# Kernel tuning notes

Measured on AMD Instinct MI355X. Metric: run time of the kernel, lower is better.

## Reference

```python
import jax, jax.numpy as jnp
import numpy as np

D_MODEL = 1024
NHEAD = 16
HEAD_DIM = D_MODEL // NHEAD


def setup_inputs() -> dict:
    key = jax.random.key(0)
    ks = jax.random.split(key, 7)
    N, S, E = 2, 2048, D_MODEL
    query = jax.random.normal(ks[0], (N, S, E), dtype=jnp.float32)
    key_t = jax.random.normal(ks[1], (N, S, E), dtype=jnp.float32)
    value = jax.random.normal(ks[2], (N, S, E), dtype=jnp.float32)
    # nn.Linear default init scale ~ 1/sqrt(fan_in)
    s = 1.0 / np.sqrt(E)
    w_in = jax.random.uniform(ks[3], (3 * E, E), jnp.float32, -s, s)
    b_in = jax.random.uniform(ks[4], (3 * E,), jnp.float32, -s, s)
    w_o = jax.random.uniform(ks[5], (E, E), jnp.float32, -s, s)
    b_o = jax.random.uniform(ks[6], (E,), jnp.float32, -s, s)
    return {"query": query, "key": key_t, "value": value,
            "w_in": w_in, "b_in": b_in, "w_o": w_o, "b_o": b_o}


def reference(query, key, value, w_in, b_in, w_o, b_o):
    # NOTE: the torch module computes q,k,v all from `query` (self-attention);
    # the `key`/`value` args are ignored by its forward math.
    N, S, E = query.shape
    H, Dh = NHEAD, HEAD_DIM
    qkv = query @ w_in.T + b_in                      # (N, S, 3E)
    q, k, v = jnp.split(qkv, 3, axis=-1)
    def heads(x):
        return x.reshape(N, S, H, Dh).transpose(0, 2, 1, 3)  # (N, H, S, Dh)
    q, k, v = heads(q), heads(k), heads(v)
    scale = 1.0 / jnp.sqrt(jnp.asarray(Dh, query.dtype))
    scores = jnp.einsum('bhqd,bhkd->bhqk', q, k) * scale     # (N, H, S, S)
    attn = jax.nn.softmax(scores, axis=-1)
    out = jnp.einsum('bhqk,bhkd->bhqd', attn, v)             # (N, H, S, Dh)
    out = out.transpose(0, 2, 1, 3).reshape(N, S, E)
    return out @ w_o.T + b_o
```

## Files before the change

### kernel.cpp

```cpp
#include <hip/hip_runtime.h>
#include <hip/hip_bf16.h>
#include <stdint.h>

#define NB   2
#define SEQ  2048
#define EMB  1024
#define NH   16
#define DH   64
#define MR   (NB*SEQ)
#define E3   (3*EMB)
#define CSC  (0.125f * 1.44269504f)

typedef __attribute__((ext_vector_type(8))) short bf16x8;
typedef __attribute__((ext_vector_type(4))) float f32x4;
typedef __attribute__((ext_vector_type(16))) float f32x16;

__device__ __forceinline__ unsigned short f2bf(float f) {
  unsigned u = __float_as_uint(f);
  unsigned r = (u + 0x7FFF + ((u >> 16) & 1)) >> 16;
  return (unsigned short)r;
}
__device__ __forceinline__ unsigned pack2(float lo, float hi) {
  return (unsigned)f2bf(lo) | ((unsigned)f2bf(hi) << 16);
}
__device__ __forceinline__ float bf2f(unsigned short s) {
  return __uint_as_float(((unsigned)s) << 16);
}
__device__ __forceinline__ unsigned cvtpk(float lo, float hi) {
  unsigned r;
  asm("v_cvt_pk_bf16_f32 %0, %1, %2" : "=v"(r) : "v"(lo), "v"(hi));
  return r;
}

__device__ __forceinline__ void gld16(const unsigned short* g, unsigned short* l) {
  __builtin_amdgcn_global_load_lds(
      (const __attribute__((address_space(1))) unsigned int*)g,
      (__attribute__((address_space(3))) unsigned int*)l,
      16, 0, 0);
}

__global__ void cvt_all(const float* __restrict__ q,
                        const float* __restrict__ w_in,
                        const float* __restrict__ w_o,
                        unsigned short* __restrict__ Xbf,
                        unsigned short* __restrict__ Winbf,
                        unsigned short* __restrict__ Wobf) {
  int b = blockIdx.x;
  const float* src; unsigned short* dst; int off;
  if (b < 2048)      { src = q;    dst = Xbf;   off = b; }
  else if (b < 3584) { src = w_in; dst = Winbf; off = b - 2048; }
  else               { src = w_o;  dst = Wobf;  off = b - 3584; }
  int i = (off * 256 + threadIdx.x) * 8;
  float4 a = *(const float4*)(src + i);
  float4 c = *(const float4*)(src + i + 4);
  uint4 o;
  o.x = pack2(a.x, a.y);
  o.y = pack2(a.z, a.w);
  o.z = pack2(c.x, c.y);
  o.w = pack2(c.z, c.w);
  *(uint4*)(dst + i) = o;
}

template<int BN, bool OUT_F32>
__global__ __launch_bounds__(256) void gemm_bt(
    const unsigned short* __restrict__ A,
    const unsigned short* __restrict__ Bt,
    const float* __restrict__ bias,
    void* __restrict__ Cout,
    int K, int ldc, int scale_cols) {
  constexpr int NR = BN / 32;
  constexpr int WNT = BN / 2;
  __shared__ unsigned short As[4096];
  __shared__ unsigned short Bs[BN * 32];
  const int tid  = threadIdx.x;
  const int lane = tid & 63;
  const int w    = tid >> 6;
  const int wm = w >> 1, wn = w & 1;
  const int g = lane >> 4, li = lane & 15;
  const int rowBase = blockIdx.x * 128;
  const int colBase = blockIdx.y * BN;

  f32x4 acc[4][NR];
#pragma unroll
  for (int m = 0; m < 4; ++m)
#pragma unroll
    for (int nn = 0; nn < NR; ++nn) { acc[m][nn][0]=0.f; acc[m][nn][1]=0.f; acc[m][nn][2]=0.f; acc[m][nn][3]=0.f; }

  const unsigned short* Ag = A  + (size_t)(rowBase + (tid >> 2)) * K + (tid & 3) * 8;
  const unsigned short* Bg = Bt + (size_t)(colBase + (tid >> 2)) * K + (tid & 3) * 8;

  for (int k0 = 0; k0 < K; k0 += 32) {
    __syncthreads();
    gld16(Ag + k0,                As + tid * 8);
    gld16(Ag + (size_t)64*K + k0, As + 2048 + tid * 8);
    gld16(Bg + k0,                Bs + tid * 8);
    if (BN == 128)
      gld16(Bg + (size_t)64*K + k0, Bs + 2048 + tid * 8);
    __syncthreads();

    bf16x8 af[4], bfv[NR];
#pragma unroll
    for (int m = 0; m < 4; ++m)
      af[m] = *(const bf16x8*)&As[(wm*64 + m*16 + li) * 32 + g * 8];
#pragma unroll
    for (int nn = 0; nn < NR; ++nn)
      bfv[nn] = *(const bf16x8*)&Bs[(wn*WNT + nn*16 + li) * 32 + g * 8];
#pragma unroll
    for (int m = 0; m < 4; ++m)
#pragma unroll
      for (int nn = 0; nn < NR; ++nn)
        acc[m][nn] = __builtin_amdgcn_mfma_f32_16x16x32_bf16(af[m], bfv[nn], acc[m][nn], 0, 0, 0);
  }

#pragma unroll
  for (int nn = 0; nn < NR; ++nn) {
    const int col = colBase + wn*WNT + nn*16 + li;
    const float bv = bias[col];
    const float sc = (col < scale_cols) ? CSC : 1.0f;
#pragma unroll
    for (int m = 0; m < 4; ++m) {
      const int r0 = rowBase + wm*64 + m*16 + g*4;
#pragma unroll
      for (int r = 0; r < 4; ++r) {
        float v = (acc[m][nn][r] + bv) * sc;
        if (OUT_F32) ((float*)Cout)[(size_t)(r0 + r) * ldc + col] = v;
        else ((unsigned short*)Cout)[(size_t)(r0 + r) * ldc + col] = f2bf(v);
      }
    }
  }
}

__global__ __launch_bounds__(256, 3) void attn32(
    const unsigned short* __restrict__ qkv,
    unsigned short* __restrict__ O0,
    unsigned short* __restrict__ O1,
    float* __restrict__ ML) {
  __shared__ unsigned short smem[16384];
  char* LB = (char*)smem;

  const int tid  = threadIdx.x;
  const int lane = tid & 63;
  const int w    = tid >> 6;
  const int hi   = lane >> 5;
  const int l31  = lane & 31;
  const int slot = blockIdx.x;
  const int bid  = (slot & 7) * 128 + (slot >> 3);
  const int qb = bid & 15, h = (bid >> 4) & 15, n = (bid >> 8) & 1, z = bid >> 9;
  const size_t rowN = (size_t)n * SEQ;
  const int kt0 = z * 1024;
  const int vp_ = tid & 31, dblk = tid >> 5;
  const int vps = (vp_ & ~6) | ((vp_ & 2) << 1) | ((vp_ & 4) >> 1);
  unsigned short* Oz = z ? O1 : O0;

  bf16x8 qf[4];
  {
    const size_t qr = rowN + qb*128 + w*32 + l31;
#pragma unroll
    for (int kc = 0; kc < 4; ++kc)
      qf[kc] = *(const bf16x8*)&qkv[qr * E3 + h*64 + kc*16 + hi*8];
  }

  f32x16 ZEROV;
#pragma unroll
  for (int i = 0; i < 16; ++i) ZEROV[i] = 0.f;
  f32x16 acc0 = ZEROV, acc1 = ZEROV;
  float ssum[8];
#pragma unroll
  for (int i = 0; i < 8; ++i) ssum[i] = 0.f;

  uint4 pv0, pv1;
  auto stageK = [&](int kt, int buf) {
#pragma unroll
    for (int p = 0; p < 2; ++p) {
      int r = p*32 + (tid >> 3);
      int ch = (tid & 7) ^ (r & 7);
      gld16(&qkv[(rowN + kt + r) * E3 + EMB + h*64 + ch*8],
            &smem[buf*4096 + p*2048 + tid*8]);
    }
  };
  auto loadV = [&](int kt) {
    const unsigned short* vp = &qkv[(rowN + kt + 2*vp_) * E3 + 2*EMB + h*64 + dblk*8];
    pv0 = *(const uint4*)vp;
    pv1 = *(const uint4*)(vp + E3);
  };
  auto writeV = [&](int buf) {
    const unsigned short* s0 = (const unsigned short*)&pv0;
    const unsigned short* s1 = (const unsigned short*)&pv1;
#pragma unroll
    for (int j = 0; j < 8; ++j) {
      int d = dblk*8 + j;
      unsigned val = (unsigned)s0[j] | ((unsigned)s1[j] << 16);
      *(unsigned*)(LB + 16384 + buf*8192 + d*128 + (((vps>>2) ^ (d&7)) << 4) + (vps&3)*4) = val;
    }
  };

  loadV(kt0);
  stageK(kt0, 0);
  writeV(0);
  __syncthreads();

  for (int t = 0; t < 16; ++t) {
    const int cur = t & 1;
    const bool pre = (t + 1 < 16);
    const int ktn = kt0 + (t + 1) * 64;
    if (pre) { loadV(ktn); stageK(ktn, cur^1); }

    const char* Kb = LB + cur*8192;
    bf16x8 ka[4], kb[4];
#pragma unroll
    for (int kc = 0; kc < 4; ++kc) {
      const int sw = ((kc*2 + hi) ^ (l31 & 7)) << 4;
      ka[kc] = *(const bf16x8*)(Kb + l31*128 + sw);
      kb[kc] = *(const bf16x8*)(Kb + 4096 + l31*128 + sw);
    }
    __builtin_amdgcn_s_setprio(1);
    f32x16 z0 = __builtin_amdgcn_mfma_f32_32x32x16_bf16(ka[0], qf[0], ZEROV, 0, 0, 0);
    f32x16 z1 = __builtin_amdgcn_mfma_f32_32x32x16_bf16(kb[0], qf[0], ZEROV, 0, 0, 0);
#pragma unroll
    for (int kc = 1; kc < 4; ++kc) {
      z0 = __builtin_amdgcn_mfma_f32_32x32x16_bf16(ka[kc], qf[kc], z0, 0, 0, 0);
      z1 = __builtin_amdgcn_mfma_f32_32x32x16_bf16(kb[kc], qf[kc], z1, 0, 0, 0);
    }
    __builtin_amdgcn_s_setprio(0);

#pragma unroll
    for (int i = 0; i < 16; ++i) {
      z0[i] = __builtin_amdgcn_exp2f(z0[i]);
      z1[i] = __builtin_amdgcn_exp2f(z1[i]);
    }
#pragma unroll
    for (int i = 0; i < 8; ++i)
      ssum[i] += (z0[2*i] + z0[2*i+1]) + (z1[2*i] + z1[2*i+1]);

    bf16x8 pf[4];
    {
      union { bf16x8 v; unsigned u[4]; } r0_, r1_, r2_, r3_;
#pragma unroll
      for (int j = 0; j < 4; ++j) {
        r0_.u[j] = cvtpk(z0[2*j],     z0[2*j + 1]);
        r1_.u[j] = cvtpk(z0[8 + 2*j], z0[9 + 2*j]);
        r2_.u[j] = cvtpk(z1[2*j],     z1[2*j + 1]);
        r3_.u[j] = cvtpk(z1[8 + 2*j], z1[9 + 2*j]);
      }
      pf[0] = r0_.v; pf[1] = r1_.v; pf[2] = r2_.v; pf[3] = r3_.v;
    }

    if (pre) writeV(cur ^ 1);

    const char* Vb = LB + 16384 + cur*8192;
    __builtin_amdgcn_s_setprio(1);
#pragma unroll
    for (int c = 0; c < 4; ++c) {
      const int sw = ((c*2 + hi) ^ (l31 & 7)) << 4;
      bf16x8 va = *(const bf16x8*)(Vb + l31*128 + sw);
      bf16x8 vb = *(const bf16x8*)(Vb + 4096 + l31*128 + sw);
      acc0 = __builtin_amdgcn_mfma_f32_32x32x16_bf16(va, pf[c], acc0, 0, 0, 0);
      acc1 = __builtin_amdgcn_mfma_f32_32x32x16_bf16(vb, pf[c], acc1, 0, 0, 0);
    }
    __builtin_amdgcn_s_setprio(0);
    __syncthreads();
  }

#pragma unroll
  for (int st = 4; st; st >>= 1)
#pragma unroll
    for (int i = 0; i < st; ++i) ssum[i] += ssum[i + st];
  float lsum = ssum[0] + __shfl_xor(ssum[0], 32);

  const int qrow_l = w*32 + l31;
  if (hi == 0) {
    size_t grow = rowN + qb*128 + qrow_l;
    ML[(size_t)z*65536 + grow*16 + h] = lsum;
  }

  float rn = 1.0f / lsum;
#pragma unroll
  for (int dt = 0; dt < 2; ++dt) {
#pragma unroll
    for (int r = 0; r < 16; r += 2) {
      float v0 = (dt ? acc1[r]   : acc0[r])   * rn;
      float v1 = (dt ? acc1[r+1] : acc0[r+1]) * rn;
      int d = dt*32 + (r & 3) + 8*(r >> 2) + 4*hi;
      unsigned val = pack2(v0, v1);
      int col32 = d >> 1;
      int g = col32 >> 2;
      *(unsigned*)(LB + qrow_l*128 + ((g ^ (qrow_l & 7)) << 4) + (col32 & 3)*4) = val;
    }
  }
  __syncthreads();
  {
    int row = tid >> 1;
    size_t orow = (rowN + qb*128 + row) * EMB + h*64;
#pragma unroll
    for (int i = 0; i < 4; ++i) {
      int gg = (tid & 1)*4 + i;
      uint4 v = *(const uint4*)(LB + row*128 + ((gg ^ (row & 7)) << 4));
      *(uint4*)&Oz[orow + gg*8] = v;
    }
  }
}

__global__ void attn_combine(const unsigned short* __restrict__ O0,
                             const unsigned short* __restrict__ O1,
                             const float* __restrict__ ML,
                             unsigned short* __restrict__ x2) {
  int idx = (blockIdx.x * 256 + threadIdx.x) * 8;
  int row = idx >> 10;
  int h = (idx & 1023) >> 6;
  float l0 = ML[row*16 + h];
  float l1 = ML[65536 + row*16 + h];
  float rl = 1.0f / (l0 + l1);
  float w0 = l0 * rl, w1 = l1 * rl;
  uint4 u0 = *(const uint4*)(O0 + idx);
  uint4 u1 = *(const uint4*)(O1 + idx);
  const unsigned* p0 = (const unsigned*)&u0;
  const unsigned* p1 = (const unsigned*)&u1;
  uint4 o;
  unsigned* po = (unsigned*)&o;
#pragma unroll
  for (int j = 0; j < 4; ++j) {
    float lo = w0 * bf2f((unsigned short)(p0[j] & 0xFFFF))
             + w1 * bf2f((unsigned short)(p1[j] & 0xFFFF));
    float hv = w0 * bf2f((unsigned short)(p0[j] >> 16))
             + w1 * bf2f((unsigned short)(p1[j] >> 16));
    po[j] = pack2(lo, hv);
  }
  *(uint4*)(x2 + idx) = o;
}

extern "C" void kernel_launch(void* const* d_in, const int* in_sizes, int n_in,
                              void* d_out, int out_size, void* d_ws, size_t ws_size,
                              hipStream_t stream) {
  const float* q    = (const float*)d_in[0];
  const float* w_in = (const float*)d_in[3];
  const float* b_in = (const float*)d_in[4];
  const float* w_o  = (const float*)d_in[5];
  const float* b_o  = (const float*)d_in[6];

  char* ws = (char*)d_ws;
  unsigned short* Wobf  = (unsigned short*)(ws);
  unsigned short* Xbf   = (unsigned short*)(ws + 2097152);
  unsigned short* Winbf = (unsigned short*)(ws + 10485760);
  unsigned short* QKV   = (unsigned short*)(ws + 16777216);
  unsigned short* X2    = (unsigned short*)(ws + 41943040);
  unsigned short* O0    = Xbf;
  unsigned short* O1    = X2;
  float*          ML    = (float*)(ws + 10485760);

  cvt_all<<<4096, 256, 0, stream>>>(q, w_in, w_o, Xbf, Winbf, Wobf);

  gemm_bt<128, false><<<dim3(32, 24), 256, 0, stream>>>(Xbf, Winbf, b_in, (void*)QKV, EMB, E3, 1024);
  attn32<<<NB * NH * (SEQ / 128) * 2, 256, 0, stream>>>(QKV, O0, O1, ML);
  attn_combine<<<2048, 256, 0, stream>>>(O0, O1, ML, X2);
  gemm_bt<64, true><<<dim3(32, 16), 256, 0, stream>>>(X2, Wobf, b_o, d_out, EMB, EMB, 0);
}
```

Baseline: 123.1 us.

## Drop split-K attention and combine kernel; each block covers full key range

The attention kernel no longer splits the key sequence into two halves. Each block now loops over all 32 key tiles and writes the normalized output straight into X2. This removes the partial-output writes, the ML sum buffer and the separate combine launch. The cost is half as many blocks (512 instead of 1024) at 3 blocks/CU, which lowers parallelism and latency hiding on a 256-CU part. The code appears to use a fixed-max softmax (sums only, no running max), so correctness is unchanged.

Measured after the change: 117.0 us. -5.0%, faster.

```diff
diff --git a/kernel.cpp b/kernel.cpp
--- a/kernel.cpp
+++ b/kernel.cpp
@@ -132,9 +132,7 @@
 
 __global__ __launch_bounds__(256, 3) void attn32(
     const unsigned short* __restrict__ qkv,
-    unsigned short* __restrict__ O0,
-    unsigned short* __restrict__ O1,
-    float* __restrict__ ML) {
+    unsigned short* __restrict__ x2) {
   __shared__ unsigned short smem[16384];
   char* LB = (char*)smem;
 
@@ -144,13 +142,11 @@
   const int hi   = lane >> 5;
   const int l31  = lane & 31;
   const int slot = blockIdx.x;
-  const int bid  = (slot & 7) * 128 + (slot >> 3);
-  const int qb = bid & 15, h = (bid >> 4) & 15, n = (bid >> 8) & 1, z = bid >> 9;
+  const int bid  = (slot & 7) * 64 + (slot >> 3);
+  const int qb = bid & 15, h = (bid >> 4) & 15, n = bid >> 8;
   const size_t rowN = (size_t)n * SEQ;
-  const int kt0 = z * 1024;
   const int vp_ = tid & 31, dblk = tid >> 5;
   const int vps = (vp_ & ~6) | ((vp_ & 2) << 1) | ((vp_ & 4) >> 1);
-  unsigned short* Oz = z ? O1 : O0;
 
   bf16x8 qf[4];
   {
@@ -194,15 +190,15 @@
     }
   };
 
-  loadV(kt0);
-  stageK(kt0, 0);
+  loadV(0);
+  stageK(0, 0);
   writeV(0);
   __syncthreads();
 
-  for (int t = 0; t < 16; ++t) {
+  for (int t = 0; t < 32; ++t) {
     const int cur = t & 1;
-    const bool pre = (t + 1 < 16);
-    const int ktn = kt0 + (t + 1) * 64;
+    const bool pre = (t + 1 < 32);
+    const int ktn = (t + 1) * 64;
     if (pre) { loadV(ktn); stageK(ktn, cur^1); }
 
     const char* Kb = LB + cur*8192;
@@ -267,13 +263,8 @@
     for (int i = 0; i < st; ++i) ssum[i] += ssum[i + st];
   float lsum = ssum[0] + __shfl_xor(ssum[0], 32);
 
+  float rn = 1.0f / lsum;
   const int qrow_l = w*32 + l31;
-  if (hi == 0) {
-    size_t grow = rowN + qb*128 + qrow_l;
-    ML[(size_t)z*65536 + grow*16 + h] = lsum;
-  }
-
-  float rn = 1.0f / lsum;
 #pragma unroll
   for (int dt = 0; dt < 2; ++dt) {
 #pragma unroll
@@ -295,37 +286,9 @@
     for (int i = 0; i < 4; ++i) {
       int gg = (tid & 1)*4 + i;
       uint4 v = *(const uint4*)(LB + row*128 + ((gg ^ (row & 7)) << 4));
-      *(uint4*)&Oz[orow + gg*8] = v;
-    }
-  }
-}
-
-__global__ void attn_combine(const unsigned short* __restrict__ O0,
-                             const unsigned short* __restrict__ O1,
-                             const float* __restrict__ ML,
-                             unsigned short* __restrict__ x2) {
-  int idx = (blockIdx.x * 256 + threadIdx.x) * 8;
-  int row = idx >> 10;
-  int h = (idx & 1023) >> 6;
-  float l0 = ML[row*16 + h];
-  float l1 = ML[65536 + row*16 + h];
-  float rl = 1.0f / (l0 + l1);
-  float w0 = l0 * rl, w1 = l1 * rl;
-  uint4 u0 = *(const uint4*)(O0 + idx);
-  uint4 u1 = *(const uint4*)(O1 + idx);
-  const unsigned* p0 = (const unsigned*)&u0;
-  const unsigned* p1 = (const unsigned*)&u1;
-  uint4 o;
-  unsigned* po = (unsigned*)&o;
-#pragma unroll
-  for (int j = 0; j < 4; ++j) {
-    float lo = w0 * bf2f((unsigned short)(p0[j] & 0xFFFF))
-             + w1 * bf2f((unsigned short)(p1[j] & 0xFFFF));
-    float hv = w0 * bf2f((unsigned short)(p0[j] >> 16))
-             + w1 * bf2f((unsigned short)(p1[j] >> 16));
-    po[j] = pack2(lo, hv);
-  }
-  *(uint4*)(x2 + idx) = o;
+      *(uint4*)&x2[orow + gg*8] = v;
+    }
+  }
 }
 
 extern "C" void kernel_launch(void* const* d_in, const int* in_sizes, int n_in,
@@ -343,14 +306,10 @@
   unsigned short* Winbf = (unsigned short*)(ws + 10485760);
   unsigned short* QKV   = (unsigned short*)(ws + 16777216);
   unsigned short* X2    = (unsigned short*)(ws + 41943040);
-  unsigned short* O0    = Xbf;
-  unsigned short* O1    = X2;
-  float*          ML    = (float*)(ws + 10485760);
 
   cvt_all<<<4096, 256, 0, stream>>>(q, w_in, w_o, Xbf, Winbf, Wobf);
 
   gemm_bt<128, false><<<dim3(32, 24), 256, 0, stream>>>(Xbf, Winbf, b_in, (void*)QKV, EMB, E3, 1024);
-  attn32<<<NB * NH * (SEQ / 128) * 2, 256, 0, stream>>>(QKV, O0, O1, ML);
-  attn_combine<<<2048, 256, 0, stream>>>(O0, O1, ML, X2);
+  attn32<<<NB * NH * (SEQ / 128), 256, 0, stream>>>(QKV, X2);
   gemm_bt<64, true><<<dim3(32, 16), 256, 0, stream>>>(X2, Wobf, b_o, d_out, EMB, EMB, 0);
 }
```
